# Performance work log

Measured on AMD Instinct MI355X. Metric: run time of the kernel, lower is better.

The kernel has to match this reference:

```python
import jax, jax.numpy as jnp
import numpy as np

B, T, D, E = 2, 8192, 256, 8
TWO_D = 2 * D
N = B * T
CAP = N // E            # expert-choice capacity per expert
PRIME_DELAYS = (1, 2, 3, 5)
LOCAL_ITERS = 8
BASE_LR = 0.5
LR_DECAY = 0.85


def setup_inputs() -> dict:
    key = jax.random.key(0)
    ks = jax.random.split(key, 6)
    x_stream = jax.random.normal(ks[0], (B, T, D, 2), jnp.float32)
    phase = jax.random.uniform(ks[1], (D,), jnp.float32) * (2.0 * np.float32(np.pi))
    cos_p = jnp.cos(phase)
    sin_p = jnp.sin(phase)
    delay_gains = jax.random.normal(ks[2], (len(PRIME_DELAYS), D, 2), jnp.float32) * 0.02
    gate_w = jax.random.normal(ks[3], (TWO_D, E), jnp.float32) * np.float32(1.0 / np.sqrt(TWO_D))
    expert_w = jax.random.normal(ks[4], (E, TWO_D, TWO_D), jnp.float32) * np.float32(1.0 / np.sqrt(TWO_D))
    act_bias = jax.random.normal(ks[5], (D, 2), jnp.float32) * 0.01
    return {"x_stream": x_stream, "delay_gains": delay_gains, "cos_p": cos_p,
            "sin_p": sin_p, "gate_w": gate_w, "expert_w": expert_w, "act_bias": act_bias}


def _phase_targets(x, cos_p, sin_p):
    # target[:,1:] = phase-rotated x[:,:-1]; target[:,0] = x[:,0]
    pr, pi = x[:, :-1, :, 0], x[:, :-1, :, 1]
    rot = jnp.stack([pr * cos_p - pi * sin_p, pr * sin_p + pi * cos_p], axis=-1)
    return jnp.concatenate([x[:, :1], rot], axis=1)


def _apply_delays(x, gains):
    # x_eff[:, tau:] += complex_mul(x[:, :-tau], gain[tau])  (reads original x)
    xe = x
    for i, tau in enumerate(PRIME_DELAYS):
        gr, gi = gains[i, :, 0], gains[i, :, 1]
        dr, di = x[:, :-tau, :, 0], x[:, :-tau, :, 1]
        upd = jnp.stack([dr * gr - di * gi, dr * gi + di * gr], axis=-1)
        xe = xe.at[:, tau:].add(upd)
    return xe


def _moe(x_eff, gate_w, expert_w):
    # Expert-choice MoE: softmax gate per token, each expert picks top-CAP tokens.
    xf = x_eff.reshape(N, TWO_D)
    scores = jax.nn.softmax(xf @ gate_w, axis=-1)          # [N, E]
    vals, idx = jax.lax.top_k(scores.T, CAP)               # [E, CAP]
    xg = xf[idx]                                           # [E, CAP, 2D]
    yo = jnp.einsum('ecd,edf->ecf', xg, expert_w)          # [E, CAP, 2D]
    flat_idx = idx.reshape(-1)
    pred = jnp.zeros((N, TWO_D), xf.dtype).at[flat_idx].add((vals[..., None] * yo).reshape(-1, TWO_D))
    counts = jnp.zeros((N,), xf.dtype).at[flat_idx].add(1.0)
    return pred.reshape(B, T, D, 2), counts


def _normalize_activate(pred, counts, act_bias):
    denom = jnp.maximum(counts, 1.0).reshape(B, T, 1, 1)
    return jnp.tanh(pred / denom + act_bias)


def reference(x_stream, delay_gains, cos_p, sin_p, gate_w, expert_w, act_bias):
    x = x_stream.astype(jnp.float32)
    x_target_frozen = _phase_targets(x, cos_p, sin_p)

    # ---- no-grad fixed-point inner loop (local_iters == min_iters == 8 => fixed 8 iters) ----
    x_states = x
    lr = BASE_LR
    pred = counts = None
    for _ in range(LOCAL_ITERS):
        x_eff = _apply_delays(x_states, delay_gains)
        pred, counts = _moe(x_eff, gate_w, expert_w)
        residual = x_target_frozen - pred
        x_states = x_states + lr * jnp.clip(residual, -10.0, 10.0)
        lr = lr * LR_DECAY
    x_states = jax.lax.stop_gradient(_normalize_activate(pred, counts, act_bias))
    x_target_ng = jax.lax.stop_gradient(x_target_frozen)

    # ---- differentiable tail ----
    x_target_grad = _phase_targets(x, cos_p, sin_p)
    x_eff_grad = _apply_delays(x_states, delay_gains)
    pred_grad, _ = _moe(x_eff_grad, gate_w, expert_w)
    out = x_states + BASE_LR * (x_target_grad - pred_grad)
    res_norm = jnp.linalg.norm(x_target_ng - pred_grad, axis=-1).mean()
    return out.astype(x_stream.dtype), res_norm
```

## Files before the change

kernel.cpp:

```cpp
#include <hip/hip_runtime.h>

#define T_    8192
#define D_    256
#define E_    8
#define TWOD  512
#define NTOK  16384
#define CAP_  2048
#define NQ    (NTOK * 128)

__global__ __launch_bounds__(256) void init_kernel(const float4* __restrict__ x,
    const float* __restrict__ cosp, const float* __restrict__ sinp,
    float4* __restrict__ xt, float4* __restrict__ xs)
{
  int q = blockIdx.x * 256 + threadIdx.x;
  int n = q >> 7, dq = q & 127, t = n & (T_ - 1);
  float4 v = x[q];
  xs[q] = v;
  float4 g;
  if (t == 0) {
    g = v;
  } else {
    float4 p = x[q - 128];
    int d0 = dq * 2;
    float c0 = cosp[d0], s0 = sinp[d0], c1 = cosp[d0 + 1], s1 = sinp[d0 + 1];
    g.x = p.x * c0 - p.y * s0;
    g.y = p.x * s0 + p.y * c0;
    g.z = p.z * c1 - p.w * s1;
    g.w = p.z * s1 + p.w * c1;
  }
  xt[q] = g;
}

__global__ __launch_bounds__(256) void delays_gate_kernel(const float4* __restrict__ xs,
    const float* __restrict__ gains, const float* __restrict__ gw,
    float4* __restrict__ xe, float* __restrict__ scoresT)
{
  int q = blockIdx.x * 256 + threadIdx.x;
  int n = q >> 7, dq = q & 127, t = n & (T_ - 1);
  float4 v = xs[q];
  const int taus[4] = {1, 2, 3, 5};
  int d0 = dq * 2;
  #pragma unroll
  for (int i = 0; i < 4; i++) {
    int tau = taus[i];
    if (t >= tau) {
      float4 p = xs[q - tau * 128];
      float gr0 = gains[(i * D_ + d0) * 2 + 0], gi0 = gains[(i * D_ + d0) * 2 + 1];
      float gr1 = gains[(i * D_ + d0 + 1) * 2 + 0], gi1 = gains[(i * D_ + d0 + 1) * 2 + 1];
      v.x += p.x * gr0 - p.y * gi0;
      v.y += p.x * gi0 + p.y * gr0;
      v.z += p.z * gr1 - p.w * gi1;
      v.w += p.z * gi1 + p.w * gr1;
    }
  }
  xe[q] = v;

  float p8[8] = {0, 0, 0, 0, 0, 0, 0, 0};
  const float4* gw4 = (const float4*)gw;
  float av[4] = {v.x, v.y, v.z, v.w};
  #pragma unroll
  for (int j = 0; j < 4; j++) {
    float4 w0 = gw4[(dq * 4 + j) * 2];
    float4 w1 = gw4[(dq * 4 + j) * 2 + 1];
    float a = av[j];
    p8[0] = fmaf(a, w0.x, p8[0]);
    p8[1] = fmaf(a, w0.y, p8[1]);
    p8[2] = fmaf(a, w0.z, p8[2]);
    p8[3] = fmaf(a, w0.w, p8[3]);
    p8[4] = fmaf(a, w1.x, p8[4]);
    p8[5] = fmaf(a, w1.y, p8[5]);
    p8[6] = fmaf(a, w1.z, p8[6]);
    p8[7] = fmaf(a, w1.w, p8[7]);
  }
  #pragma unroll
  for (int off = 32; off > 0; off >>= 1)
    #pragma unroll
    for (int e = 0; e < 8; e++) p8[e] += __shfl_down(p8[e], off);
  __shared__ float red[4][8];
  int wv = threadIdx.x >> 6;
  if ((threadIdx.x & 63) == 0)
    #pragma unroll
    for (int e = 0; e < 8; e++) red[wv][e] = p8[e];
  __syncthreads();
  if (threadIdx.x < 2) {
    int tok = blockIdx.x * 2 + threadIdx.x;
    float pe[8], m = -1e30f;
    #pragma unroll
    for (int e = 0; e < 8; e++) {
      pe[e] = red[threadIdx.x * 2][e] + red[threadIdx.x * 2 + 1][e];
      m = fmaxf(m, pe[e]);
    }
    float ssum = 0.f;
    #pragma unroll
    for (int e = 0; e < 8; e++) { pe[e] = expf(pe[e] - m); ssum += pe[e]; }
    float inv = 1.0f / ssum;
    #pragma unroll
    for (int e = 0; e < 8; e++) scoresT[e * NTOK + tok] = pe[e] * inv;
  }
}

__global__ __launch_bounds__(1024) void select_kernel(const float* __restrict__ scoresT,
    int* __restrict__ idxl, int* __restrict__ slot_of)
{
  int e = blockIdx.x;
  const float* s = scoresT + (size_t)e * NTOK;
  int tid = threadIdx.x;
  int lane = tid & 63, wv = tid >> 6;

  float4 f[4];
  #pragma unroll
  for (int j = 0; j < 4; j++) f[j] = ((const float4*)s)[tid + 1024 * j];
  unsigned uv[16];
  #pragma unroll
  for (int j = 0; j < 4; j++) {
    uv[j * 4 + 0] = __float_as_uint(f[j].x);
    uv[j * 4 + 1] = __float_as_uint(f[j].y);
    uv[j * 4 + 2] = __float_as_uint(f[j].z);
    uv[j * 4 + 3] = __float_as_uint(f[j].w);
  }

  __shared__ int hist[16][257];
  __shared__ int histsum[256];
  __shared__ int sfx[2][256];
  __shared__ int wsum[16], wpre[16];
  __shared__ int shB, shK, shTot, scnt;

  unsigned prefix = 0;
  int k = CAP_;
  for (int p = 0; p < 4; ++p) {
    int shift = 24 - 8 * p;
    for (int b = tid; b < 16 * 257; b += 1024) ((int*)hist)[b] = 0;
    __syncthreads();
    #pragma unroll
    for (int r = 0; r < 16; r++) {
      unsigned u = uv[r];
      bool match = (p == 0) || ((u >> (shift + 8)) == prefix);
      if (match) atomicAdd(&hist[wv][(u >> shift) & 255], 1);
    }
    __syncthreads();
    if (tid < 256) {
      int tsum = 0;
      #pragma unroll
      for (int w = 0; w < 16; w++) tsum += hist[w][tid];
      histsum[tid] = tsum;
      sfx[0][tid] = tsum;
    }
    __syncthreads();
    int cur = 0;
    #pragma unroll
    for (int d = 1; d < 256; d <<= 1) {
      if (tid < 256)
        sfx[cur ^ 1][tid] = sfx[cur][tid] + ((tid + d < 256) ? sfx[cur][tid + d] : 0);
      __syncthreads();
      cur ^= 1;
    }
    if (tid < 256) {
      int sv = sfx[cur][tid];
      int snext = (tid < 255) ? sfx[cur][tid + 1] : 0;
      if (sv >= k && snext < k) { shB = tid; shK = k - snext; }
    }
    __syncthreads();
    prefix = (prefix << 8) | (unsigned)shB;
    k = shK;
    __syncthreads();
  }
  unsigned thr = prefix;
  int kk = k;

  if (tid == 0) scnt = 0;
  __syncthreads();
  int jb = 0;
  #pragma unroll
  for (int j = 0; j < 4; j++) {
    int eqf[4], c = 0;
    #pragma unroll
    for (int cc = 0; cc < 4; cc++) {
      eqf[cc] = (uv[j * 4 + cc] == thr) ? 1 : 0;
      c += eqf[cc];
    }
    int sc = c;
    #pragma unroll
    for (int d = 1; d < 64; d <<= 1) {
      int tt = __shfl_up(sc, d);
      if (lane >= d) sc += tt;
    }
    if (lane == 63) wsum[wv] = sc;
    __syncthreads();
    if (tid == 0) {
      int a = 0;
      #pragma unroll
      for (int w = 0; w < 16; w++) { int t2 = wsum[w]; wpre[w] = a; a += t2; }
      shTot = a;
    }
    __syncthreads();
    int excl = wpre[wv] + (sc - c);
    int local = 0;
    int sov[4];
    #pragma unroll
    for (int cc = 0; cc < 4; cc++) {
      unsigned u = uv[j * 4 + cc];
      int n = 4 * tid + 4096 * j + cc;
      bool take = (u > thr) || (eqf[cc] && (jb + excl + local) < kk);
      local += eqf[cc];
      unsigned long long msk = __ballot(take);
      int cntw = __popcll(msk);
      int base = 0;
      if (lane == 0 && cntw) base = atomicAdd(&scnt, cntw);
      base = __shfl(base, 0);
      int slot = base + __popcll(msk & ((1ull << lane) - 1ull));
      int sv = -1;
      if (take) {
        idxl[e * CAP_ + slot] = n;
        sv = slot;
      }
      sov[cc] = sv;
    }
    int4 so;
    so.x = sov[0]; so.y = sov[1]; so.z = sov[2]; so.w = sov[3];
    ((int4*)(slot_of + (size_t)e * NTOK))[tid + 1024 * j] = so;
    jb += shTot;
    __syncthreads();
  }
}

#define GM 128
#define GN 128
#define GKK 32
__device__ __forceinline__ float comp4(const float4 v, int u) {
  return u == 0 ? v.x : u == 1 ? v.y : u == 2 ? v.z : v.w;
}
__global__ __launch_bounds__(256) void gemm_kernel(const float* __restrict__ xe,
    const float* __restrict__ ew, const int* __restrict__ idxl, float* __restrict__ yo)
{
  int bid0 = blockIdx.x;
  int bid = (bid0 & 7) * 64 + (bid0 >> 3);
  int e = bid >> 6, rem = bid & 63, mt = rem >> 2, nt = rem & 3;
  __shared__ float4 As4[GM * 8];
  __shared__ float4 Bs4[GKK * 32];
  __shared__ int rowtok[GM];
  int tid = threadIdx.x;
  if (tid < GM) rowtok[tid] = idxl[e * CAP_ + mt * GM + tid];
  __syncthreads();
  int tx = tid & 15, ty = tid >> 4;
  const float* We = ew + (size_t)e * TWOD * TWOD + nt * GN;
  float acc[8][8] = {};

  for (int kb = 0; kb < TWOD; kb += GKK) {
    #pragma unroll
    for (int l = 0; l < 4; l++) {
      int id = tid + l * 256;
      int row = id >> 3, kq = id & 7;
      float4 a = *(const float4*)(xe + (size_t)rowtok[row] * TWOD + kb + kq * 4);
      As4[row * 8 + (kq ^ ((row >> 3) & 7))] = a;
      int kkk = id >> 5, cc = id & 31;
      float4 b = *(const float4*)(We + (size_t)(kb + kkk) * TWOD + cc * 4);
      Bs4[kkk * 32 + cc] = b;
    }
    __syncthreads();
    #pragma unroll
    for (int k4 = 0; k4 < GKK; k4 += 4) {
      int kq = k4 >> 2;
      float4 a4[8], b4[8];
      #pragma unroll
      for (int i = 0; i < 8; i++) a4[i] = As4[(ty * 8 + i) * 8 + (kq ^ (ty & 7))];
      #pragma unroll
      for (int u = 0; u < 4; u++) {
        b4[2 * u]     = Bs4[(k4 + u) * 32 + tx];
        b4[2 * u + 1] = Bs4[(k4 + u) * 32 + 16 + tx];
      }
      #pragma unroll
      for (int u = 0; u < 4; u++) {
        float av[8], bv[8];
        #pragma unroll
        for (int i = 0; i < 8; i++) av[i] = comp4(a4[i], u);
        bv[0] = b4[2*u].x; bv[1] = b4[2*u].y; bv[2] = b4[2*u].z; bv[3] = b4[2*u].w;
        bv[4] = b4[2*u+1].x; bv[5] = b4[2*u+1].y; bv[6] = b4[2*u+1].z; bv[7] = b4[2*u+1].w;
        #pragma unroll
        for (int i = 0; i < 8; i++)
          #pragma unroll
          for (int jj = 0; jj < 8; jj++)
            acc[i][jj] = fmaf(av[i], bv[jj], acc[i][jj]);
      }
    }
    __syncthreads();
  }
  #pragma unroll
  for (int i = 0; i < 8; i++) {
    float* dst = yo + (size_t)(e * CAP_ + mt * GM + ty * 8 + i) * TWOD + nt * GN + tx * 4;
    float4 o0 = {acc[i][0], acc[i][1], acc[i][2], acc[i][3]};
    float4 o1 = {acc[i][4], acc[i][5], acc[i][6], acc[i][7]};
    *(float4*)dst = o0;
    *(float4*)(dst + 64) = o1;
  }
}

__global__ __launch_bounds__(256) void combine_update_kernel(const float4* __restrict__ yo,
    const float* __restrict__ scoresT, const int* __restrict__ slot_of,
    const float4* __restrict__ xt, float4* __restrict__ xs,
    float4* __restrict__ pred, int* __restrict__ counts, float lr, int write_pred)
{
  int q = blockIdx.x * 256 + threadIdx.x;
  int n = q >> 7, dq = q & 127;
  float4 p = {0, 0, 0, 0};
  int cnt = 0;
  #pragma unroll
  for (int e = 0; e < E_; e++) {
    int sl = slot_of[e * NTOK + n];
    if (sl >= 0) {
      float val = scoresT[e * NTOK + n];
      float4 y = yo[(size_t)(e * CAP_ + sl) * 128 + dq];
      p.x = fmaf(val, y.x, p.x);
      p.y = fmaf(val, y.y, p.y);
      p.z = fmaf(val, y.z, p.z);
      p.w = fmaf(val, y.w, p.w);
      cnt++;
    }
  }
  float4 t = xt[q], s = xs[q];
  s.x += lr * fminf(fmaxf(t.x - p.x, -10.f), 10.f);
  s.y += lr * fminf(fmaxf(t.y - p.y, -10.f), 10.f);
  s.z += lr * fminf(fmaxf(t.z - p.z, -10.f), 10.f);
  s.w += lr * fminf(fmaxf(t.w - p.w, -10.f), 10.f);
  xs[q] = s;
  if (write_pred) {
    pred[q] = p;
    if (dq == 0) counts[n] = cnt;
  }
}

__global__ __launch_bounds__(256) void combine_final_kernel(const float4* __restrict__ yo,
    const float* __restrict__ scoresT, const int* __restrict__ slot_of,
    const float4* __restrict__ xt, const float4* __restrict__ xs,
    float4* __restrict__ out, float* __restrict__ racc)
{
  int q = blockIdx.x * 256 + threadIdx.x;
  int n = q >> 7, dq = q & 127;
  float4 p = {0, 0, 0, 0};
  #pragma unroll
  for (int e = 0; e < E_; e++) {
    int sl = slot_of[e * NTOK + n];
    if (sl >= 0) {
      float val = scoresT[e * NTOK + n];
      float4 y = yo[(size_t)(e * CAP_ + sl) * 128 + dq];
      p.x = fmaf(val, y.x, p.x);
      p.y = fmaf(val, y.y, p.y);
      p.z = fmaf(val, y.z, p.z);
      p.w = fmaf(val, y.w, p.w);
    }
  }
  float4 t = xt[q], s = xs[q];
  float dr0 = t.x - p.x, di0 = t.y - p.y, dr1 = t.z - p.z, di1 = t.w - p.w;
  float4 o = {s.x + 0.5f * dr0, s.y + 0.5f * di0, s.z + 0.5f * dr1, s.w + 0.5f * di1};
  out[q] = o;
  float lsum = sqrtf(dr0 * dr0 + di0 * di0) + sqrtf(dr1 * dr1 + di1 * di1);
  __shared__ float red[256];
  red[threadIdx.x] = lsum;
  __syncthreads();
  for (int off = 128; off > 0; off >>= 1) {
    if (threadIdx.x < off) red[threadIdx.x] += red[threadIdx.x + off];
    __syncthreads();
  }
  if (threadIdx.x == 0) atomicAdd(racc, red[0]);
}

__global__ __launch_bounds__(256) void activate_kernel(const float4* __restrict__ pred,
    const int* __restrict__ counts, const float4* __restrict__ bias, float4* __restrict__ xs)
{
  int q = blockIdx.x * 256 + threadIdx.x;
  int n = q >> 7;
  float denom = fmaxf((float)counts[n], 1.0f);
  float4 p = pred[q];
  float4 b = bias[q & 127];
  float4 r;
  r.x = tanhf(p.x / denom + b.x);
  r.y = tanhf(p.y / denom + b.y);
  r.z = tanhf(p.z / denom + b.z);
  r.w = tanhf(p.w / denom + b.w);
  xs[q] = r;
}

__global__ void finish_kernel(const float* __restrict__ racc, float* __restrict__ dst)
{
  if (threadIdx.x == 0) dst[0] = racc[0] / 4194304.0f;
}

extern "C" void kernel_launch(void* const* d_in, const int* in_sizes, int n_in,
                              void* d_out, int out_size, void* d_ws, size_t ws_size,
                              hipStream_t stream)
{
  const float* x     = (const float*)d_in[0];
  const float* gains = (const float*)d_in[1];
  const float* cosp  = (const float*)d_in[2];
  const float* sinp  = (const float*)d_in[3];
  const float* gw    = (const float*)d_in[4];
  const float* ew    = (const float*)d_in[5];
  const float* bias  = (const float*)d_in[6];
  float* out = (float*)d_out;

  char* w = (char*)d_ws;
  size_t off = 0;
  auto alloc = [&](size_t bytes) -> void* {
    void* p = w + off;
    off += (bytes + 255) & ~(size_t)255;
    return p;
  };
  float* xt      = (float*)alloc((size_t)NTOK * TWOD * 4);
  float* xs      = (float*)alloc((size_t)NTOK * TWOD * 4);
  float* xe      = (float*)alloc((size_t)NTOK * TWOD * 4);
  float* pred    = (float*)alloc((size_t)NTOK * TWOD * 4);
  float* yo      = (float*)alloc((size_t)E_ * CAP_ * TWOD * 4);
  float* scoresT = (float*)alloc((size_t)E_ * NTOK * 4);
  int*   idxl    = (int*)  alloc((size_t)E_ * CAP_ * 4);
  int*   slot_of = (int*)  alloc((size_t)E_ * NTOK * 4);
  int*   counts  = (int*)  alloc((size_t)NTOK * 4);
  float* racc    = (float*)alloc(256);

  const int eb = NQ / 256;

  init_kernel<<<eb, 256, 0, stream>>>((const float4*)x, cosp, sinp, (float4*)xt, (float4*)xs);

  double lr = 0.5;
  for (int it = 0; it < 9; ++it) {
    if (it == 8)
      activate_kernel<<<eb, 256, 0, stream>>>((const float4*)pred, counts,
                                              (const float4*)bias, (float4*)xs);
    delays_gate_kernel<<<eb, 256, 0, stream>>>((const float4*)xs, gains, gw,
                                               (float4*)xe, scoresT);
    select_kernel<<<E_, 1024, 0, stream>>>(scoresT, idxl, slot_of);
    gemm_kernel<<<512, 256, 0, stream>>>(xe, ew, idxl, yo);
    if (it < 8) {
      combine_update_kernel<<<eb, 256, 0, stream>>>((const float4*)yo, scoresT, slot_of,
          (const float4*)xt, (float4*)xs, (float4*)pred, counts, (float)lr, it == 7 ? 1 : 0);
      lr *= 0.85;
    } else {
      hipMemsetAsync(racc, 0, 4, stream);
      combine_final_kernel<<<eb, 256, 0, stream>>>((const float4*)yo, scoresT, slot_of,
          (const float4*)xt, (const float4*)xs, (float4*)out, racc);
    }
  }
  finish_kernel<<<1, 64, 0, stream>>>(racc, out + (size_t)NTOK * TWOD);
}
```

Measured before the change: 1.900 ms.

## Double-buffer GEMM tiles with direct global-to-LDS async loads

The expert GEMM kernel now loads its A and B tiles straight from global memory into LDS with global_load_lds instead of going through registers. The shared buffers are doubled so the next K tile can be fetched while the current one is being computed. The per-thread gather pointers for routed token rows are computed once up front, which also drops the rowtok shared array. The cost is twice the LDS per block, which may lower occupancy, and the change relies on wave-level LDS write placement to keep the XOR-swizzled layout correct.

```diff
diff --git a/kernel.cpp b/kernel.cpp
--- a/kernel.cpp
+++ b/kernel.cpp
@@ -229,34 +229,56 @@
 __device__ __forceinline__ float comp4(const float4 v, int u) {
   return u == 0 ? v.x : u == 1 ? v.y : u == 2 ? v.z : v.w;
 }
+__device__ __forceinline__ void gl_lds16(const void* g, void* l) {
+  __builtin_amdgcn_global_load_lds(
+      (const __attribute__((address_space(1))) unsigned int*)g,
+      (__attribute__((address_space(3))) unsigned int*)l, 16, 0, 0);
+}
 __global__ __launch_bounds__(256) void gemm_kernel(const float* __restrict__ xe,
     const float* __restrict__ ew, const int* __restrict__ idxl, float* __restrict__ yo)
 {
   int bid0 = blockIdx.x;
   int bid = (bid0 & 7) * 64 + (bid0 >> 3);
   int e = bid >> 6, rem = bid & 63, mt = rem >> 2, nt = rem & 3;
-  __shared__ float4 As4[GM * 8];
-  __shared__ float4 Bs4[GKK * 32];
-  __shared__ int rowtok[GM];
+  __shared__ float4 AB[2 * 2048];
   int tid = threadIdx.x;
-  if (tid < GM) rowtok[tid] = idxl[e * CAP_ + mt * GM + tid];
-  __syncthreads();
   int tx = tid & 15, ty = tid >> 4;
   const float* We = ew + (size_t)e * TWOD * TWOD + nt * GN;
+
+  const float* aptr0[4];
+  const float* bptr0[4];
+  #pragma unroll
+  for (int l = 0; l < 4; l++) {
+    int slot = l * 256 + tid;
+    int row = slot >> 3, kqs = slot & 7;
+    int kq = kqs ^ ((row >> 3) & 7);
+    int tok = idxl[e * CAP_ + mt * GM + row];
+    aptr0[l] = xe + (size_t)tok * TWOD + kq * 4;
+    int kkk = slot >> 5, cc = slot & 31;
+    bptr0[l] = We + (size_t)kkk * TWOD + cc * 4;
+  }
+  int wbase = tid & 192;
+
+  auto stage = [&](int buf, int kb) {
+    float4* dA = AB + buf * 2048 + wbase;
+    float4* dB = dA + 1024;
+    #pragma unroll
+    for (int l = 0; l < 4; l++) {
+      gl_lds16(aptr0[l] + kb, (void*)(dA + l * 256));
+      gl_lds16(bptr0[l] + (size_t)kb * TWOD, (void*)(dB + l * 256));
+    }
+  };
+
+  stage(0, 0);
+  __syncthreads();
+
   float acc[8][8] = {};
-
-  for (int kb = 0; kb < TWOD; kb += GKK) {
-    #pragma unroll
-    for (int l = 0; l < 4; l++) {
-      int id = tid + l * 256;
-      int row = id >> 3, kq = id & 7;
-      float4 a = *(const float4*)(xe + (size_t)rowtok[row] * TWOD + kb + kq * 4);
-      As4[row * 8 + (kq ^ ((row >> 3) & 7))] = a;
-      int kkk = id >> 5, cc = id & 31;
-      float4 b = *(const float4*)(We + (size_t)(kb + kkk) * TWOD + cc * 4);
-      Bs4[kkk * 32 + cc] = b;
-    }
-    __syncthreads();
+  int cur = 0;
+
+  for (int kb = GKK; kb <= TWOD; kb += GKK) {
+    if (kb < TWOD) stage(cur ^ 1, kb);
+    const float4* As4 = AB + cur * 2048;
+    const float4* Bs4 = As4 + 1024;
     #pragma unroll
     for (int k4 = 0; k4 < GKK; k4 += 4) {
       int kq = k4 >> 2;
@@ -283,7 +305,9 @@
       }
     }
     __syncthreads();
-  }
+    cur ^= 1;
+  }
+
   #pragma unroll
   for (int i = 0; i < 8; i++) {
     float* dst = yo + (size_t)(e * CAP_ + mt * GM + ty * 8 + i) * TWOD + nt * GN + tx * 4;
```

Measured after the change: 2.103 ms. 10.7% more time.
